# Kernel tuning notes

Measured on AMD Instinct MI355X. Metric: run time of the kernel, lower is better.

## Reference

```python
import jax, jax.numpy as jnp
import numpy as np

B, T, C, H = 2, 2048, 2048, 16
HD = C // H  # 128
WINDOW = 2048


def setup_inputs() -> dict:
    key = jax.random.key(0)
    k0, k1, k2 = jax.random.split(key, 3)
    s = 0.02  # GPT-2 style init scale
    return {
        "x": jax.random.normal(k0, (B, T, C), jnp.float32),
        "w_attn": jax.random.normal(k1, (3 * C, C), jnp.float32) * s,
        "b_attn": jnp.zeros((3 * C,), jnp.float32),
        "w_proj": jax.random.normal(k2, (C, C), jnp.float32) * s,
        "b_proj": jnp.zeros((C,), jnp.float32),
    }


def reference(x, w_attn, b_attn, w_proj, b_proj):
    Bb, Tt, Cc = x.shape
    # fused qkv projection (torch Linear: y = x @ W^T + b)
    qkv = x @ w_attn.T + b_attn                       # [B, T, 3C]
    q, k, v = jnp.split(qkv, 3, axis=2)

    def to_heads(t):
        return t.reshape(Bb, Tt, H, HD).transpose(0, 2, 1, 3)  # [B, H, T, HD]

    q, k, v = to_heads(q), to_heads(k), to_heads(v)
    K = k.shape[2]  # kv length (== T, no past_kv)

    attn = jnp.einsum('bhqd,bhkd->bhqk', q, k) / jnp.sqrt(jnp.float32(HD))
    # Faithful to source: mask[:, :, T-1:T, :K] — single tril row T-1 broadcast
    # over all query positions (for prefill K==T this row is all ones).
    mask_row = jnp.arange(K) <= (Tt - 1)              # [K] bool
    attn = jnp.where(mask_row[None, None, None, :], attn, -jnp.inf)
    weights = jax.nn.softmax(attn, axis=-1)            # [B, H, T, K]
    # dropout p=0.0 (eval): identity
    ctx = jnp.einsum('bhqk,bhkd->bhqd', weights, v)    # [B, H, T, HD]
    ctx = ctx.transpose(0, 2, 1, 3).reshape(Bb, Tt, Cc)
    out = ctx @ w_proj.T + b_proj                      # [B, T, C]
    return (out, k, v)  # (context, present_kv)
```

## Files before the change

### kernel.cpp

```cpp
#include <hip/hip_runtime.h>
#include <hip/hip_bf16.h>
#include <cstdint>
#include <cstddef>
#include <cmath>

typedef __attribute__((ext_vector_type(8))) short short8;
typedef __attribute__((ext_vector_type(4))) short bf16x4;
typedef __attribute__((ext_vector_type(4))) float f32x4;

static constexpr int BB = 2, T = 2048, C = 2048, H = 16, HD = 128;
static constexpr int M = BB * T;
static constexpr size_t BTC = (size_t)BB * T * C;

__device__ __forceinline__ short f2bf(float f) {
    union { float f; uint32_t u; } v; v.f = f;
    uint32_t u = v.u;
    uint32_t r = (u + 0x7fffu + ((u >> 16) & 1u)) >> 16;
    return (short)r;
}

__device__ __forceinline__ short f2bf_fast(float f) {
    __hip_bfloat16 h = __float2bfloat16(f);
    return *reinterpret_cast<short*>(&h);
}

__device__ __forceinline__ void gl_lds16(const void* g, void* l) {
    __builtin_amdgcn_global_load_lds(
        (const __attribute__((address_space(1))) unsigned int*)g,
        (__attribute__((address_space(3))) unsigned int*)l, 16, 0, 0);
}

__global__ void cvt_all_in(const float* __restrict__ x, const float* __restrict__ wa,
                           const float* __restrict__ wp,
                           short* __restrict__ xb, short* __restrict__ wab,
                           short* __restrict__ wpb) {
    int i = (blockIdx.x * 256 + threadIdx.x) * 8;
    const float* src;
    short* dst;
    if (i < (int)BTC) { src = x + i; dst = xb + i; }
    else if (i < (int)(BTC + 12582912)) { src = wa + (i - (int)BTC); dst = wab + (i - (int)BTC); }
    else { src = wp + (i - (int)(BTC + 12582912)); dst = wpb + (i - (int)(BTC + 12582912)); }
    float4 a = *(const float4*)(src);
    float4 b = *(const float4*)(src + 4);
    short8 o;
    o[0] = f2bf(a.x); o[1] = f2bf(a.y); o[2] = f2bf(a.z); o[3] = f2bf(a.w);
    o[4] = f2bf(b.x); o[5] = f2bf(b.y); o[6] = f2bf(b.z); o[7] = f2bf(b.w);
    *(short8*)(dst) = o;
}

__launch_bounds__(512, 2)
__global__ void gemm_qkv8p(const short* __restrict__ A, const short* __restrict__ Bw,
                           const float* __restrict__ bias, float* __restrict__ outF,
                           short* __restrict__ q_ws, short* __restrict__ k_ws) {
    extern __shared__ char lds[];
    constexpr int K = 2048, NKT = K / 64;
    constexpr int BUFSZ = 57344;

    int bid = blockIdx.x;
    int g = bid & 7, j = bid >> 3;
    int by = (g & 1) * 8 + (j >> 3);
    int bx = (g >> 1) * 8 + (j & 7);
    int row0 = by * 256, col0 = bx * 192;

    int t = threadIdx.x, w = t >> 6, l = t & 63;
    int lr = l & 15, lg = l >> 4;
    int wr = w >> 2, wc = w & 3;

    const char* srcb[7];
    int dstoff[7];
#pragma unroll
    for (int c = 0; c < 7; c++) {
        bool isA = c < 4;
        int coff = (isA ? c : c - 4) * 8192 + t * 16;
        int row = coff >> 7;
        int colb = (coff & 127) ^ ((row & 7) << 4);
        srcb[c] = isA ? (const char*)A + (size_t)(row0 + row) * (K * 2) + colb
                      : (const char*)Bw + (size_t)(col0 + row) * (K * 2) + colb;
        dstoff[c] = (isA ? 0 : 32768) + coff;
    }

    f32x4 acc[8][3] = {};

    auto ST = [&](int c, int kt) {
        gl_lds16(srcb[c] + kt * 128, lds + (kt & 1) * BUFSZ + dstoff[c]);
    };
    auto RD_A = [&](const char* Ab, int ks, int mih, short8* af) {
#pragma unroll
        for (int mi2 = 0; mi2 < 4; mi2++) {
            int row = wr * 128 + mih * 64 + mi2 * 16 + lr;
            af[mi2] = *(const short8*)(Ab + row * 128 +
                       ((ks * 64 + lg * 16) ^ ((row & 7) << 4)));
        }
    };
    auto RD_B = [&](const char* Bb, int ks, short8* bfr) {
#pragma unroll
        for (int ni = 0; ni < 3; ni++) {
            int row = wc * 48 + ni * 16 + lr;
            bfr[ni] = *(const short8*)(Bb + row * 128 +
                       ((ks * 64 + lg * 16) ^ ((row & 7) << 4)));
        }
    };
    auto MM = [&](short8* af, short8* bfr, int mih) {
        __builtin_amdgcn_s_setprio(1);
#pragma unroll
        for (int mi2 = 0; mi2 < 4; mi2++)
#pragma unroll
            for (int ni = 0; ni < 3; ni++)
                acc[mih * 4 + mi2][ni] = __builtin_amdgcn_mfma_f32_16x16x32_bf16(
                    af[mi2], bfr[ni], acc[mih * 4 + mi2][ni], 0, 0, 0);
        __builtin_amdgcn_s_setprio(0);
    };

#pragma unroll
    for (int c = 0; c < 7; c++) ST(c, 0);
    ST(0, 1); ST(2, 1);
    asm volatile("s_waitcnt vmcnt(2)" ::: "memory");
    __builtin_amdgcn_s_barrier();

    for (int it = 0; it < NKT / 2; ++it) {
        int ta = 2 * it, tb = ta + 1;
        const char* A0 = lds;          const char* B0 = lds + 32768;
        const char* A1 = lds + BUFSZ;  const char* B1 = lds + BUFSZ + 32768;
        bool s2 = (ta + 2 < NKT), s3 = (tb + 2 < NKT);
        short8 af[4], bfr[3];

        RD_A(A0, 0, 0, af); RD_B(B0, 0, bfr);
        ST(1, tb); ST(3, tb);
        __builtin_amdgcn_s_barrier();
        MM(af, bfr, 0);
        __builtin_amdgcn_s_barrier();

        RD_A(A0, 0, 1, af);
        ST(4, tb); ST(5, tb);
        __builtin_amdgcn_s_barrier();
        MM(af, bfr, 1);
        __builtin_amdgcn_s_barrier();

        RD_A(A0, 1, 0, af); RD_B(B0, 1, bfr);
        ST(6, tb);
        __builtin_amdgcn_s_barrier();
        MM(af, bfr, 0);
        __builtin_amdgcn_s_barrier();

        RD_A(A0, 1, 1, af);
        if (s2) {
            ST(0, ta + 2); ST(2, ta + 2);
            asm volatile("s_waitcnt vmcnt(2)" ::: "memory");
        } else {
            asm volatile("s_waitcnt vmcnt(0)" ::: "memory");
        }
        __builtin_amdgcn_s_barrier();
        MM(af, bfr, 1);
        __builtin_amdgcn_s_barrier();

        RD_A(A1, 0, 0, af); RD_B(B1, 0, bfr);
        if (s2) { ST(1, ta + 2); ST(3, ta + 2); }
        __builtin_amdgcn_s_barrier();
        MM(af, bfr, 0);
        __builtin_amdgcn_s_barrier();

        RD_A(A1, 0, 1, af);
        if (s2) { ST(4, ta + 2); ST(5, ta + 2); }
        __builtin_amdgcn_s_barrier();
        MM(af, bfr, 1);
        __builtin_amdgcn_s_barrier();

        RD_A(A1, 1, 0, af); RD_B(B1, 1, bfr);
        if (s2) ST(6, ta + 2);
        __builtin_amdgcn_s_barrier();
        MM(af, bfr, 0);
        __builtin_amdgcn_s_barrier();

        RD_A(A1, 1, 1, af);
        if (s3) {
            ST(0, tb + 2); ST(2, tb + 2);
            asm volatile("s_waitcnt vmcnt(2)" ::: "memory");
        } else {
            asm volatile("s_waitcnt vmcnt(0)" ::: "memory");
        }
        __builtin_amdgcn_s_barrier();
        MM(af, bfr, 1);
        __builtin_amdgcn_s_barrier();
    }

    const float SCF = 0.12753123813884803f;
#pragma unroll
    for (int mi = 0; mi < 8; mi++) {
        int gr0 = row0 + wr * 128 + mi * 16 + lg * 4;
#pragma unroll
        for (int ni = 0; ni < 3; ni++) {
            int gc = col0 + wc * 48 + ni * 16 + lr;
            float bv = bias[gc];
            int sec = gc >> 11, cc = gc & 2047;
            int h = cc >> 7, d = cc & 127;
#pragma unroll
            for (int r = 0; r < 4; r++) {
                float val = acc[mi][ni][r] + bv;
                int gr = gr0 + r;
                int b = gr >> 11, tt = gr & 2047;
                size_t idx = ((size_t)(b * H + h) * T + tt) * HD + d;
                if (sec == 0) {
                    q_ws[idx] = f2bf(val * SCF);
                } else if (sec == 1) {
                    outF[BTC + idx] = val;
                    k_ws[idx] = f2bf(val);
                } else {
                    outF[2 * BTC + idx] = val;
                }
            }
        }
    }
}

template<int NI, int EPI, int NBX>
__launch_bounds__(512, 2)
__global__ void gemm8p(const short* __restrict__ A, const short* __restrict__ Bw,
                       const float* __restrict__ bias, float* __restrict__ outF,
                       int Ndim) {
    extern __shared__ char lds[];
    constexpr int K = 2048, NKT = K / 64;
    constexpr int NCH = 4 + NI;
    constexpr int BUFSZ = 32768 + NI * 8192;

    int bid = blockIdx.x;
    int nwg = gridDim.x;
    int swz = (bid & 7) * (nwg >> 3) + (bid >> 3);
    int by = swz / NBX, bx = swz % NBX;
    int row0 = by * 256, col0 = bx * (NI * 64);

    int t = threadIdx.x, w = t >> 6, l = t & 63;
    int lr = l & 15, lg = l >> 4;
    int wr = w >> 2, wc = w & 3;

    const char* srcb[NCH];
    int dstoff[NCH];
#pragma unroll
    for (int c = 0; c < NCH; c++) {
        bool isA = c < 4;
        int coff = (isA ? c : c - 4) * 8192 + t * 16;
        int row = coff >> 7;
        int colb = (coff & 127) ^ ((row & 7) << 4);
        srcb[c] = isA ? (const char*)A + (size_t)(row0 + row) * (K * 2) + colb
                      : (const char*)Bw + (size_t)(col0 + row) * (K * 2) + colb;
        dstoff[c] = (isA ? 0 : 32768) + coff;
    }

    f32x4 acc[8][NI] = {};

#pragma unroll
    for (int c = 0; c < NCH; c++) gl_lds16(srcb[c], lds + dstoff[c]);
#pragma unroll
    for (int c = 0; c < NCH; c++) gl_lds16(srcb[c] + 128, lds + BUFSZ + dstoff[c]);
    asm volatile("s_waitcnt vmcnt(%0)" :: "n"(NCH) : "memory");
    __builtin_amdgcn_s_barrier();

    for (int kt = 0; kt < NKT; kt++) {
        char* base = lds + (kt & 1) * BUFSZ;
        const char* Bbase = base + 32768;
        int koff = (kt + 2) * 128;
        bool pf = (kt + 2 < NKT);

        short8 bfr[NI][2];
#pragma unroll
        for (int p = 0; p < 4; p++) {
            short8 af[2][2];
#pragma unroll
            for (int mi2 = 0; mi2 < 2; mi2++) {
                int row = wr * 128 + p * 32 + mi2 * 16 + lr;
#pragma unroll
                for (int ks = 0; ks < 2; ks++)
                    af[mi2][ks] = *(const short8*)(base + row * 128 +
                                  ((ks * 64 + lg * 16) ^ ((row & 7) << 4)));
            }
            if (p == 0) {
#pragma unroll
                for (int ni = 0; ni < NI; ni++) {
                    int row = wc * (NI * 16) + ni * 16 + lr;
#pragma unroll
                    for (int ks = 0; ks < 2; ks++)
                        bfr[ni][ks] = *(const short8*)(Bbase + row * 128 +
                                      ((ks * 64 + lg * 16) ^ ((row & 7) << 4)));
                }
            }
            __builtin_amdgcn_s_barrier();
            __builtin_amdgcn_s_setprio(1);
#pragma unroll
            for (int ks = 0; ks < 2; ks++)
#pragma unroll
                for (int mi2 = 0; mi2 < 2; mi2++)
#pragma unroll
                    for (int ni = 0; ni < NI; ni++)
                        acc[p * 2 + mi2][ni] = __builtin_amdgcn_mfma_f32_16x16x32_bf16(
                            af[mi2][ks], bfr[ni][ks], acc[p * 2 + mi2][ni], 0, 0, 0);
            __builtin_amdgcn_s_setprio(0);
            __builtin_amdgcn_s_barrier();

            if (p == 0 && pf) {
#pragma unroll
                for (int c = 4; c < NCH; c++) gl_lds16(srcb[c] + koff, base + dstoff[c]);
            }
            if (p == 1 && pf) {
                gl_lds16(srcb[0] + koff, base + dstoff[0]);
                gl_lds16(srcb[2] + koff, base + dstoff[2]);
            }
            if (p == 3) {
                if (pf) {
                    gl_lds16(srcb[1] + koff, base + dstoff[1]);
                    gl_lds16(srcb[3] + koff, base + dstoff[3]);
                    asm volatile("s_waitcnt vmcnt(%0)" :: "n"(NCH) : "memory");
                } else {
                    asm volatile("s_waitcnt vmcnt(0)" ::: "memory");
                }
                __builtin_amdgcn_s_barrier();
            }
        }
    }

#pragma unroll
    for (int mi = 0; mi < 8; mi++) {
        int gr0 = row0 + wr * 128 + mi * 16 + lg * 4;
#pragma unroll
        for (int ni = 0; ni < NI; ni++) {
            int gc = col0 + wc * (NI * 16) + ni * 16 + lr;
            float bv = bias[gc];
#pragma unroll
            for (int r = 0; r < 4; r++)
                outF[(size_t)(gr0 + r) * Ndim + gc] = acc[mi][ni][r] + bv;
        }
    }
}

__global__ void vtrans(const float* __restrict__ vin, short* __restrict__ vT) {
    __shared__ float tile[64 * 65];
    int blk = blockIdx.x;
    int bh = blk >> 6, rem = blk & 63;
    int t0 = (rem >> 1) * 64, d0 = (rem & 1) * 64;
    const float* src = vin + (size_t)bh * T * HD;
    short* dst = vT + (size_t)bh * HD * T;
    int t = threadIdx.x;
#pragma unroll
    for (int i = 0; i < 16; i++) {
        int idx = i * 256 + t;
        int r = idx >> 6, c = idx & 63;
        tile[r * 65 + c] = src[(size_t)(t0 + r) * HD + d0 + c];
    }
    __syncthreads();
#pragma unroll
    for (int i = 0; i < 16; i++) {
        int idx = i * 256 + t;
        int rd = idx >> 6, cc = idx & 63;
        dst[(size_t)(d0 + rd) * T + t0 + cc] = f2bf(tile[cc * 65 + rd]);
    }
}

__launch_bounds__(256, 2)
__global__ void attn_fwd(const short* __restrict__ q_ws, const short* __restrict__ k_ws,
                         const short* __restrict__ vT_ws, short* __restrict__ ctx) {
    __shared__ __attribute__((aligned(16))) char K_lds[2][64 * 256];
    __shared__ __attribute__((aligned(16))) char VT_lds[2][128 * 128];
    __shared__ __attribute__((aligned(16))) char P_lds[4][2][16 * 128];

    int bid = blockIdx.x;
    int blk = (bid & 7) * 64 + (bid >> 3);
    int bh = blk >> 4;
    int q0 = (blk & 15) * 128;
    int b = bh >> 4, h = bh & 15;
    int t = threadIdx.x, w = t >> 6, l = t & 63;
    int lr = l & 15, lg = l >> 4;
    int sw = (lr & 7) << 4;

    short8 qf[2][4];
#pragma unroll
    for (int qt = 0; qt < 2; qt++) {
        const short* Qp = q_ws + ((size_t)bh * T + q0 + w * 32 + qt * 16 + lr) * HD;
#pragma unroll
        for (int c = 0; c < 4; c++) qf[qt][c] = *(const short8*)(Qp + c * 32 + lg * 8);
    }

    const char* Kp = (const char*)(k_ws + (size_t)bh * T * HD);
    const short* VTp = vT_ws + (size_t)bh * HD * T;

    float lsum[2] = {0.f, 0.f};
    f32x4 acc[2][8] = {};

    auto STAGE = [&](int kt, int bsel) {
#pragma unroll
        for (int i = 0; i < 4; i++) {
            int off = i * 4096 + t * 16;
            int swzK = off ^ (((off >> 8) & 7) << 4);
            gl_lds16(Kp + (size_t)kt * 16384 + swzK, K_lds[bsel] + off);
            int swzV = off ^ (((off >> 7) & 7) << 4);
            int row = swzV >> 7, cole = (swzV & 127) >> 1;
            gl_lds16(VTp + (size_t)row * T + kt * 64 + cole, VT_lds[bsel] + off);
        }
    };

    STAGE(0, 0);
    asm volatile("s_waitcnt vmcnt(0)" ::: "memory");
    __syncthreads();

    for (int kt = 0; kt < T / 64; kt++) {
        int cur = kt & 1;
        if (kt + 1 < T / 64) STAGE(kt + 1, cur ^ 1);
        const char* Kc = K_lds[cur];
        const char* Vc = VT_lds[cur];

        f32x4 sacc[2][4] = {};
#pragma unroll
        for (int c = 0; c < 4; c++) {
#pragma unroll
            for (int kj = 0; kj < 4; kj++) {
                short8 kf = *(const short8*)(Kc + (((kj * 16 + lr) * 256 + c * 64 + lg * 16) ^ sw));
                sacc[0][kj] = __builtin_amdgcn_mfma_f32_16x16x32_bf16(kf, qf[0][c], sacc[0][kj], 0, 0, 0);
                sacc[1][kj] = __builtin_amdgcn_mfma_f32_16x16x32_bf16(kf, qf[1][c], sacc[1][kj], 0, 0, 0);
            }
        }

#pragma unroll
        for (int qt = 0; qt < 2; qt++) {
            char* Pc = P_lds[w][qt];
            float s0 = 0.f;
#pragma unroll
            for (int kj = 0; kj < 4; kj++) {
                bf16x4 pk;
#pragma unroll
                for (int r = 0; r < 4; r++) {
                    float pv = __builtin_exp2f(sacc[qt][kj][r]);
                    s0 += pv;
                    pk[r] = f2bf_fast(pv);
                }
                *(bf16x4*)(Pc + ((lr * 128 + kj * 32 + lg * 8) ^ sw)) = pk;
            }
            lsum[qt] += s0;
        }
        asm volatile("s_waitcnt lgkmcnt(0)" ::: "memory");

#pragma unroll
        for (int c2 = 0; c2 < 2; c2++) {
            short8 pf0 = *(const short8*)(P_lds[w][0] + ((lr * 128 + c2 * 64 + lg * 16) ^ sw));
            short8 pf1 = *(const short8*)(P_lds[w][1] + ((lr * 128 + c2 * 64 + lg * 16) ^ sw));
#pragma unroll
            for (int nj = 0; nj < 8; nj++) {
                short8 vf = *(const short8*)(Vc + (((nj * 16 + lr) * 128 + c2 * 64 + lg * 16) ^ sw));
                acc[0][nj] = __builtin_amdgcn_mfma_f32_16x16x32_bf16(pf0, vf, acc[0][nj], 0, 0, 0);
                acc[1][nj] = __builtin_amdgcn_mfma_f32_16x16x32_bf16(pf1, vf, acc[1][nj], 0, 0, 0);
            }
        }

        asm volatile("s_waitcnt vmcnt(0)" ::: "memory");
        __syncthreads();
    }

#pragma unroll
    for (int qt = 0; qt < 2; qt++) {
        lsum[qt] += __shfl_xor(lsum[qt], 16);
        lsum[qt] += __shfl_xor(lsum[qt], 32);
    }
#pragma unroll
    for (int qt = 0; qt < 2; qt++)
#pragma unroll
        for (int r = 0; r < 4; r++) {
            float rs = __shfl(lsum[qt], lg * 4 + r);
            float inv = 1.0f / rs;
            int tq = q0 + w * 32 + qt * 16 + lg * 4 + r;
            size_t base = ((size_t)b * T + tq) * C + h * HD;
#pragma unroll
            for (int nj = 0; nj < 8; nj++)
                ctx[base + nj * 16 + lr] = f2bf_fast(acc[qt][nj][r] * inv);
        }
}

extern "C" void kernel_launch(void* const* d_in, const int* in_sizes, int n_in,
                              void* d_out, int out_size, void* d_ws, size_t ws_size,
                              hipStream_t stream) {
    const float* x      = (const float*)d_in[0];
    const float* w_attn = (const float*)d_in[1];
    const float* b_attn = (const float*)d_in[2];
    const float* w_proj = (const float*)d_in[3];
    const float* b_proj = (const float*)d_in[4];
    float* out = (float*)d_out;

    char* ws = (char*)d_ws;
    short* x_bf  = (short*)ws;
    short* wa_bf = (short*)(ws + 16777216);
    short* ctx   = (short*)(ws + 16777216);
    short* vT    = (short*)(ws + 41943040);
    short* wp_bf = (short*)(ws + 58720256);

    short* q_ws = (short*)d_out;
    short* k_ws = (short*)d_out + BTC;

    hipFuncSetAttribute((const void*)gemm_qkv8p,
                        hipFuncAttributeMaxDynamicSharedMemorySize, 114688);
    hipFuncSetAttribute((const void*)gemm8p<2, 1, 16>,
                        hipFuncAttributeMaxDynamicSharedMemorySize, 98304);

    cvt_all_in<<<12288, 256, 0, stream>>>(x, w_attn, w_proj, x_bf, wa_bf, wp_bf);

    gemm_qkv8p<<<512, 512, 114688, stream>>>(x_bf, wa_bf, b_attn, out, q_ws, k_ws);

    vtrans<<<2048, 256, 0, stream>>>(out + 2 * BTC, vT);

    attn_fwd<<<512, 256, 0, stream>>>(q_ws, k_ws, vT, ctx);

    gemm8p<2, 1, 16><<<256, 512, 98304, stream>>>(ctx, wp_bf, b_proj, out, 2048);
}
```

Baseline: 268.2 us.

## Specialize projection GEMM with finer-grained load/compute interleave and tile swizzle

Replaces the templated projection GEMM with a dedicated kernel that processes two K-tiles per iteration. Each tile is split into smaller quarter-steps: LDS fragment reads happen per k-substep and per half of the M rows, and global-to-LDS prefetch chunks are spread across those quarter-steps. It also changes the block-to-tile mapping to a grouped 2x4 swizzle aimed at better L2 reuse. The goal is to overlap memory traffic with MFMA work more evenly. The cost is many more barriers per iteration and a more fragile waitcnt schedule.

```diff
diff --git a/kernel.cpp b/kernel.cpp
--- a/kernel.cpp
+++ b/kernel.cpp
@@ -212,30 +212,27 @@
     }
 }
 
-template<int NI, int EPI, int NBX>
 __launch_bounds__(512, 2)
-__global__ void gemm8p(const short* __restrict__ A, const short* __restrict__ Bw,
-                       const float* __restrict__ bias, float* __restrict__ outF,
-                       int Ndim) {
+__global__ void gemm_proj8p(const short* __restrict__ A, const short* __restrict__ Bw,
+                            const float* __restrict__ bias, float* __restrict__ outF) {
     extern __shared__ char lds[];
     constexpr int K = 2048, NKT = K / 64;
-    constexpr int NCH = 4 + NI;
-    constexpr int BUFSZ = 32768 + NI * 8192;
+    constexpr int BUFSZ = 49152;
 
     int bid = blockIdx.x;
-    int nwg = gridDim.x;
-    int swz = (bid & 7) * (nwg >> 3) + (bid >> 3);
-    int by = swz / NBX, bx = swz % NBX;
-    int row0 = by * 256, col0 = bx * (NI * 64);
+    int g = bid & 7, j = bid >> 3;
+    int by = (g & 1) * 8 + (j >> 2);
+    int bx = (g >> 1) * 4 + (j & 3);
+    int row0 = by * 256, col0 = bx * 128;
 
     int t = threadIdx.x, w = t >> 6, l = t & 63;
     int lr = l & 15, lg = l >> 4;
     int wr = w >> 2, wc = w & 3;
 
-    const char* srcb[NCH];
-    int dstoff[NCH];
-#pragma unroll
-    for (int c = 0; c < NCH; c++) {
+    const char* srcb[6];
+    int dstoff[6];
+#pragma unroll
+    for (int c = 0; c < 6; c++) {
         bool isA = c < 4;
         int coff = (isA ? c : c - 4) * 8192 + t * 16;
         int row = coff >> 7;
@@ -245,87 +242,111 @@
         dstoff[c] = (isA ? 0 : 32768) + coff;
     }
 
-    f32x4 acc[8][NI] = {};
-
-#pragma unroll
-    for (int c = 0; c < NCH; c++) gl_lds16(srcb[c], lds + dstoff[c]);
-#pragma unroll
-    for (int c = 0; c < NCH; c++) gl_lds16(srcb[c] + 128, lds + BUFSZ + dstoff[c]);
-    asm volatile("s_waitcnt vmcnt(%0)" :: "n"(NCH) : "memory");
+    f32x4 acc[8][2] = {};
+
+    auto ST = [&](int c, int kt) {
+        gl_lds16(srcb[c] + kt * 128, lds + (kt & 1) * BUFSZ + dstoff[c]);
+    };
+    auto RD_A = [&](const char* Ab, int ks, int mih, short8* af) {
+#pragma unroll
+        for (int mi2 = 0; mi2 < 4; mi2++) {
+            int row = wr * 128 + mih * 64 + mi2 * 16 + lr;
+            af[mi2] = *(const short8*)(Ab + row * 128 +
+                       ((ks * 64 + lg * 16) ^ ((row & 7) << 4)));
+        }
+    };
+    auto RD_B = [&](const char* Bb, int ks, short8* bfr) {
+#pragma unroll
+        for (int ni = 0; ni < 2; ni++) {
+            int row = wc * 32 + ni * 16 + lr;
+            bfr[ni] = *(const short8*)(Bb + row * 128 +
+                       ((ks * 64 + lg * 16) ^ ((row & 7) << 4)));
+        }
+    };
+    auto MM = [&](short8* af, short8* bfr, int mih) {
+        __builtin_amdgcn_s_setprio(1);
+#pragma unroll
+        for (int mi2 = 0; mi2 < 4; mi2++)
+#pragma unroll
+            for (int ni = 0; ni < 2; ni++)
+                acc[mih * 4 + mi2][ni] = __builtin_amdgcn_mfma_f32_16x16x32_bf16(
+                    af[mi2], bfr[ni], acc[mih * 4 + mi2][ni], 0, 0, 0);
+        __builtin_amdgcn_s_setprio(0);
+    };
+
+#pragma unroll
+    for (int c = 0; c < 6; c++) ST(c, 0);
+    ST(0, 1); ST(2, 1);
+    asm volatile("s_waitcnt vmcnt(2)" ::: "memory");
     __builtin_amdgcn_s_barrier();
 
-    for (int kt = 0; kt < NKT; kt++) {
-        char* base = lds + (kt & 1) * BUFSZ;
-        const char* Bbase = base + 32768;
-        int koff = (kt + 2) * 128;
-        bool pf = (kt + 2 < NKT);
-
-        short8 bfr[NI][2];
-#pragma unroll
-        for (int p = 0; p < 4; p++) {
-            short8 af[2][2];
-#pragma unroll
-            for (int mi2 = 0; mi2 < 2; mi2++) {
-                int row = wr * 128 + p * 32 + mi2 * 16 + lr;
-#pragma unroll
-                for (int ks = 0; ks < 2; ks++)
-                    af[mi2][ks] = *(const short8*)(base + row * 128 +
-                                  ((ks * 64 + lg * 16) ^ ((row & 7) << 4)));
-            }
-            if (p == 0) {
-#pragma unroll
-                for (int ni = 0; ni < NI; ni++) {
-                    int row = wc * (NI * 16) + ni * 16 + lr;
-#pragma unroll
-                    for (int ks = 0; ks < 2; ks++)
-                        bfr[ni][ks] = *(const short8*)(Bbase + row * 128 +
-                                      ((ks * 64 + lg * 16) ^ ((row & 7) << 4)));
-                }
-            }
-            __builtin_amdgcn_s_barrier();
-            __builtin_amdgcn_s_setprio(1);
-#pragma unroll
-            for (int ks = 0; ks < 2; ks++)
-#pragma unroll
-                for (int mi2 = 0; mi2 < 2; mi2++)
-#pragma unroll
-                    for (int ni = 0; ni < NI; ni++)
-                        acc[p * 2 + mi2][ni] = __builtin_amdgcn_mfma_f32_16x16x32_bf16(
-                            af[mi2][ks], bfr[ni][ks], acc[p * 2 + mi2][ni], 0, 0, 0);
-            __builtin_amdgcn_s_setprio(0);
-            __builtin_amdgcn_s_barrier();
-
-            if (p == 0 && pf) {
-#pragma unroll
-                for (int c = 4; c < NCH; c++) gl_lds16(srcb[c] + koff, base + dstoff[c]);
-            }
-            if (p == 1 && pf) {
-                gl_lds16(srcb[0] + koff, base + dstoff[0]);
-                gl_lds16(srcb[2] + koff, base + dstoff[2]);
-            }
-            if (p == 3) {
-                if (pf) {
-                    gl_lds16(srcb[1] + koff, base + dstoff[1]);
-                    gl_lds16(srcb[3] + koff, base + dstoff[3]);
-                    asm volatile("s_waitcnt vmcnt(%0)" :: "n"(NCH) : "memory");
-                } else {
-                    asm volatile("s_waitcnt vmcnt(0)" ::: "memory");
-                }
-                __builtin_amdgcn_s_barrier();
-            }
-        }
+    for (int it = 0; it < NKT / 2; ++it) {
+        int ta = 2 * it, tb = ta + 1;
+        const char* A0 = lds;          const char* B0 = lds + 32768;
+        const char* A1 = lds + BUFSZ;  const char* B1 = lds + BUFSZ + 32768;
+        bool s2 = (ta + 2 < NKT), s3 = (tb + 2 < NKT);
+        short8 af[4], bfr[2];
+
+        RD_A(A0, 0, 0, af); RD_B(B0, 0, bfr);
+        ST(1, tb); ST(3, tb);
+        __builtin_amdgcn_s_barrier();
+        MM(af, bfr, 0);
+        __builtin_amdgcn_s_barrier();
+        RD_A(A0, 0, 1, af);
+        ST(4, tb); ST(5, tb);
+        __builtin_amdgcn_s_barrier();
+        MM(af, bfr, 1);
+        __builtin_amdgcn_s_barrier();
+        RD_A(A0, 1, 0, af); RD_B(B0, 1, bfr);
+        __builtin_amdgcn_s_barrier();
+        MM(af, bfr, 0);
+        __builtin_amdgcn_s_barrier();
+        RD_A(A0, 1, 1, af);
+        if (s2) {
+            ST(0, ta + 2); ST(2, ta + 2);
+            asm volatile("s_waitcnt vmcnt(2)" ::: "memory");
+        } else {
+            asm volatile("s_waitcnt vmcnt(0)" ::: "memory");
+        }
+        __builtin_amdgcn_s_barrier();
+        MM(af, bfr, 1);
+        __builtin_amdgcn_s_barrier();
+        RD_A(A1, 0, 0, af); RD_B(B1, 0, bfr);
+        if (s2) { ST(1, ta + 2); ST(3, ta + 2); }
+        __builtin_amdgcn_s_barrier();
+        MM(af, bfr, 0);
+        __builtin_amdgcn_s_barrier();
+        RD_A(A1, 0, 1, af);
+        if (s2) { ST(4, ta + 2); ST(5, ta + 2); }
+        __builtin_amdgcn_s_barrier();
+        MM(af, bfr, 1);
+        __builtin_amdgcn_s_barrier();
+        RD_A(A1, 1, 0, af); RD_B(B1, 1, bfr);
+        __builtin_amdgcn_s_barrier();
+        MM(af, bfr, 0);
+        __builtin_amdgcn_s_barrier();
+        RD_A(A1, 1, 1, af);
+        if (s3) {
+            ST(0, tb + 2); ST(2, tb + 2);
+            asm volatile("s_waitcnt vmcnt(2)" ::: "memory");
+        } else {
+            asm volatile("s_waitcnt vmcnt(0)" ::: "memory");
+        }
+        __builtin_amdgcn_s_barrier();
+        MM(af, bfr, 1);
+        __builtin_amdgcn_s_barrier();
     }
 
 #pragma unroll
     for (int mi = 0; mi < 8; mi++) {
         int gr0 = row0 + wr * 128 + mi * 16 + lg * 4;
 #pragma unroll
-        for (int ni = 0; ni < NI; ni++) {
-            int gc = col0 + wc * (NI * 16) + ni * 16 + lr;
+        for (int ni = 0; ni < 2; ni++) {
+            int gc = col0 + wc * 32 + ni * 16 + lr;
             float bv = bias[gc];
 #pragma unroll
             for (int r = 0; r < 4; r++)
-                outF[(size_t)(gr0 + r) * Ndim + gc] = acc[mi][ni][r] + bv;
+                outF[(size_t)(gr0 + r) * 2048 + gc] = acc[mi][ni][r] + bv;
         }
     }
 }
@@ -492,7 +513,7 @@
 
     hipFuncSetAttribute((const void*)gemm_qkv8p,
                         hipFuncAttributeMaxDynamicSharedMemorySize, 114688);
-    hipFuncSetAttribute((const void*)gemm8p<2, 1, 16>,
+    hipFuncSetAttribute((const void*)gemm_proj8p,
                         hipFuncAttributeMaxDynamicSharedMemorySize, 98304);
 
     cvt_all_in<<<12288, 256, 0, stream>>>(x, w_attn, w_proj, x_bf, wa_bf, wp_bf);
@@ -503,5 +524,5 @@
 
     attn_fwd<<<512, 256, 0, stream>>>(q_ws, k_ws, vT, ctx);
 
-    gemm8p<2, 1, 16><<<256, 512, 98304, stream>>>(ctx, wp_bf, b_proj, out, 2048);
-}
+    gemm_proj8p<<<256, 512, 98304, stream>>>(ctx, wp_bf, b_proj, out);
+}
```

Result: no change. 264.2 us (-1.5%).
